# Performance work log

Measured on AMD Instinct MI355X. Metric: run time of the kernel, lower is better.

## Reference

```python
import jax, jax.numpy as jnp
import numpy as np

N_ATOMS = 8000
N_PAIRS = 80000
NF_IN = 32
NF_OUT = 32
N_DIST = 16
N_COMP = 4      # l_max=1: [l=0 (1), l=1 (3)] tensor components
N_INV = 2       # _invariant_counts[(2, 1)]
MIND_SOFT = 0.85
MAXD_SOFT = 5.0
HARD_CUTOFF = 6.5
GN_EPS = 1e-5


def _sensitivity(dist, mu, sigma):
    # HIP-NN style inverse-distance Gaussians with smooth cos^2 cutoff.
    inv_d = 1.0 / dist                                   # (P,)
    base = jnp.exp(-0.5 * ((inv_d[:, None] - mu) / sigma) ** 2)  # (P, n_dist)
    cut = jnp.where(dist < HARD_CUTOFF,
                    jnp.cos(0.5 * jnp.pi * dist / HARD_CUTOFF) ** 2, 0.0)
    return base * cut[:, None]


def setup_inputs() -> dict:
    key = jax.random.key(0)
    ks = jax.random.split(key, 10)
    in_features = jax.random.normal(ks[0], (N_ATOMS, NF_IN), jnp.float32)
    pair_first = jnp.sort(jax.random.randint(ks[1], (N_PAIRS,), 0, N_ATOMS))
    pair_second = jax.random.randint(ks[2], (N_PAIRS,), 0, N_ATOMS)
    dist_pairs = (0.5 + (HARD_CUTOFF - 0.5)
                  * jax.random.uniform(ks[3], (N_PAIRS,), jnp.float32))
    tensor_rhats = jax.random.normal(ks[4], (N_PAIRS, N_COMP), jnp.float32)
    # learned params
    sens_mu = jnp.linspace(1.0 / MAXD_SOFT, 1.0 / MIND_SOFT, N_DIST).astype(jnp.float32)
    sens_sigma = jnp.full((N_DIST,), float(sens_mu[1] - sens_mu[0]), jnp.float32)
    s_int = (2.0 / (N_DIST * NF_IN + NF_OUT)) ** 0.5
    int_weights = s_int * jax.random.normal(ks[5], (N_DIST, NF_OUT, NF_IN), jnp.float32)
    s_self = (2.0 / (NF_IN + NF_OUT)) ** 0.5
    selfint_w = s_self * jax.random.normal(ks[6], (NF_OUT, NF_IN), jnp.float32)
    selfint_b = jnp.zeros((NF_OUT,), jnp.float32)
    s_mix = (2.0 / (N_INV * NF_OUT + NF_OUT)) ** 0.5
    mixing_weights = s_mix * jax.random.normal(ks[7], (NF_OUT, N_INV, NF_OUT), jnp.float32)
    gn_weight = jnp.ones((N_INV * NF_OUT,), jnp.float32)
    gn_bias = jnp.zeros((N_INV * NF_OUT,), jnp.float32)
    return {
        "in_features": in_features, "tensor_rhats": tensor_rhats,
        "dist_pairs": dist_pairs, "int_weights": int_weights,
        "selfint_w": selfint_w, "selfint_b": selfint_b,
        "mixing_weights": mixing_weights, "gn_weight": gn_weight,
        "gn_bias": gn_bias, "sens_mu": sens_mu, "sens_sigma": sens_sigma,
        "pair_first": pair_first, "pair_second": pair_second,
    }


def reference(in_features, tensor_rhats, dist_pairs, int_weights,
              selfint_w, selfint_b, mixing_weights, gn_weight, gn_bias,
              sens_mu, sens_sigma, pair_first, pair_second):
    n_atoms = in_features.shape[0]
    # self interaction (Linear)
    self_part = in_features @ selfint_w.T + selfint_b          # (N, nf_out)
    # tensor sensitivities: (P, n_comp, n_dist) -> flat (P, n_comp*n_dist)
    sense = _sensitivity(dist_pairs, sens_mu, sens_sigma)      # (P, n_dist)
    sense_flat = (tensor_rhats[:, :, None] * sense[:, None, :]).reshape(
        -1, N_COMP * N_DIST)
    # envsum: env[a, s, f] = sum_{p: pair_first[p]=a} sense_flat[p, s] * feat[pair_second[p], f]
    feat_j = in_features[pair_second]                          # (P, nf_in)
    contrib = sense_flat[:, :, None] * feat_j[:, None, :]      # (P, S, nf_in)
    env = jax.ops.segment_sum(contrib, pair_first, num_segments=n_atoms)
    # interaction weights contraction
    w_rs = jnp.transpose(int_weights, (0, 2, 1)).reshape(N_DIST * NF_IN, NF_OUT)
    env_rs = env.reshape(n_atoms * N_COMP, N_DIST * NF_IN)
    tf = (env_rs @ w_rs).reshape(n_atoms, N_COMP, NF_OUT)
    tf = jnp.transpose(tf, (0, 2, 1))                          # (N, nf_out, n_comp)
    # HopInvariantLayer (n_max=2, l_max=1): [l=0 scalar, |l=1 vector|^2]
    invariants = jnp.stack(
        [tf[..., 0], jnp.sum(tf[..., 1:] ** 2, axis=-1)], axis=-1)  # (N, nf_out, 2)
    # GroupNorm over channels (n_inv groups of nf_out channels)
    x = jnp.transpose(invariants, (0, 2, 1))                   # (N, n_inv, nf_out)
    mean = jnp.mean(x, axis=-1, keepdims=True)
    var = jnp.var(x, axis=-1, keepdims=True)
    xn = (x - mean) / jnp.sqrt(var + GN_EPS)
    xn = xn * gn_weight.reshape(N_INV, NF_OUT) + gn_bias.reshape(N_INV, NF_OUT)
    norm_inv = jnp.transpose(xn, (0, 2, 1)).reshape(n_atoms, NF_OUT * N_INV)
    mix = norm_inv @ mixing_weights.reshape(NF_OUT * N_INV, NF_OUT)
    return mix + self_part
```

## Files before the change

kernel.cpp:

```cpp
#include <hip/hip_runtime.h>
#include <hip/hip_bf16.h>
#include <stdint.h>

#define GN_EPS 1e-5f

typedef __fp16 half2_t __attribute__((ext_vector_type(2)));
typedef __fp16 v8h __attribute__((ext_vector_type(8)));
typedef float v4f __attribute__((ext_vector_type(4)));
union U32H2 { uint32_t u; half2_t h; };
union U4V8 { uint4 u; v8h h; };

__device__ __forceinline__ float ldin(const void* p, int i, bool bf) {
    if (bf) {
        uint32_t u = (uint32_t)((const uint16_t*)p)[i];
        union { uint32_t u; float f; } c; c.u = u << 16;
        return c.f;
    }
    return ((const float*)p)[i];
}

__device__ __forceinline__ uint16_t f2bf(float x) {
    union { float f; uint32_t u; } c; c.f = x;
    uint32_t u = c.u;
    return (uint16_t)((u + 0x7FFFu + ((u >> 16) & 1u)) >> 16);
}

__device__ __forceinline__ bool detect_bf16(const void* gnw) {
    uint32_t det = *(const uint32_t*)gnw;
    return (det >> 16) == (det & 0xFFFFu);
}

__device__ __forceinline__ uint32_t pkh2(float lo, float hi) {
    U32H2 u; u.h = __builtin_amdgcn_cvt_pkrtz(lo, hi); return u.u;
}

__global__ __launch_bounds__(256) void k0_prep(
    const void* __restrict__ feat, const void* __restrict__ rhats,
    const void* __restrict__ dists, const void* __restrict__ intw,
    const void* __restrict__ selfw, const void* __restrict__ selfb,
    const void* __restrict__ mw, const void* __restrict__ gnw,
    const void* __restrict__ gnb, const void* __restrict__ mu,
    const void* __restrict__ sig, const int* __restrict__ pf,
    const int* __restrict__ ps,
    int* __restrict__ seg, uint32_t* __restrict__ Wmf,
    float* __restrict__ featf, float4* __restrict__ rc4,
    float2* __restrict__ dj2, float* __restrict__ mwf,
    float* __restrict__ selfwf, float* __restrict__ gnwf,
    float* __restrict__ gnbf, float* __restrict__ selfbf,
    float* __restrict__ muf, float* __restrict__ isgf,
    int n_atoms, int n_pairs)
{
    const bool bf = detect_bf16(gnw);
    const int tid = blockIdx.x * 256 + threadIdx.x;

    if (tid < n_pairs) {
        int a0 = pf[tid];
        if (tid == 0) { for (int a = 0; a <= a0; ++a) seg[a] = 0; }
        if (tid + 1 < n_pairs) {
            int a1 = pf[tid + 1];
            for (int a = a0 + 1; a <= a1; ++a) seg[a] = tid + 1;
        } else {
            for (int a = a0 + 1; a <= n_atoms; ++a) seg[a] = n_pairs;
        }
        float dist = ldin(dists, tid, bf);
        float cd = __cosf(0.2416609733530613f * dist);
        float cut = (dist < 6.5f) ? cd * cd : 0.0f;
        float4 rc;
        rc.x = ldin(rhats, 4 * tid + 0, bf) * cut;
        rc.y = ldin(rhats, 4 * tid + 1, bf) * cut;
        rc.z = ldin(rhats, 4 * tid + 2, bf) * cut;
        rc.w = ldin(rhats, 4 * tid + 3, bf) * cut;
        rc4[tid] = rc;
        float2 dj; dj.x = 1.0f / dist; dj.y = __int_as_float(ps[tid]);
        dj2[tid] = dj;
    }
    {
        int i0 = tid * 4;
#pragma unroll
        for (int k = 0; k < 4; ++k) {
            int i = i0 + k;
            if (i < n_atoms * 32) featf[i] = ldin(feat, i, bf);
        }
    }
    if (tid < 8192) {
        int fp = tid & 15, d = (tid >> 4) & 15, o = tid >> 8;
        float wlo = ldin(intw, (d * 32 + o) * 32 + 2 * fp, bf);
        float whi = ldin(intw, (d * 32 + o) * 32 + 2 * fp + 1, bf);
        Wmf[tid] = pkh2(wlo, whi);
    }
    if (tid < 2048) mwf[tid] = ldin(mw, tid, bf);
    if (tid < 1024) selfwf[tid] = ldin(selfw, tid, bf);
    if (tid < 64) { gnwf[tid] = ldin(gnw, tid, bf); gnbf[tid] = ldin(gnb, tid, bf); }
    if (tid < 32) selfbf[tid] = ldin(selfb, tid, bf);
    if (tid < 16) { muf[tid] = ldin(mu, tid, bf); isgf[tid] = 1.0f / ldin(sig, tid, bf); }
}

__global__ __launch_bounds__(256, 4) void k2_main(
    const int* __restrict__ seg, const uint32_t* __restrict__ Wmf,
    const float* __restrict__ featf, const float4* __restrict__ rc4,
    const float2* __restrict__ dj2, const float* __restrict__ mwf,
    const float* __restrict__ selfwf, const float* __restrict__ gnwf,
    const float* __restrict__ gnbf, const float* __restrict__ selfbf,
    const float* __restrict__ muf, const float* __restrict__ isgf,
    const void* __restrict__ gnw, void* __restrict__ out, int n_atoms)
{
    __shared__ uint32_t envs[16 * 256];
    __shared__ float tfs[4 * 32 * 4];

    const int t = threadIdx.x, wv = t >> 6, lane = t & 63;
    int a = blockIdx.x * 4 + wv;
    const bool astore = (a < n_atoms);
    if (!astore) a = n_atoms - 1;

    const int dD = lane >> 2, fq = lane & 3;
    const float mu_d = muf[dD], isg_d = isgf[dD];

    float env[4][8];
#pragma unroll
    for (int c = 0; c < 4; ++c)
#pragma unroll
        for (int fl = 0; fl < 8; ++fl) env[c][fl] = 0.0f;

    const int s = seg[a], e = seg[a + 1];

    for (int p = s; p < e; p += 4) {
        float2 dj[4]; float4 rc[4];
#pragma unroll
        for (int i = 0; i < 4; ++i) {
            int pi = (p + i < e) ? p + i : e - 1;
            dj[i] = dj2[pi];
            float4 r = rc4[pi];
            if (p + i >= e) r = make_float4(0.f, 0.f, 0.f, 0.f);
            rc[i] = r;
        }
        float4 fa[4], fb[4];
#pragma unroll
        for (int i = 0; i < 4; ++i) {
            const float4* fr = (const float4*)(featf +
                (size_t)__float_as_int(dj[i].y) * 32) + fq * 2;
            fa[i] = fr[0]; fb[i] = fr[1];
        }
#pragma unroll
        for (int i = 0; i < 4; ++i) {
            float x = (dj[i].x - mu_d) * isg_d;
            float sd = __expf(-0.5f * x * x);
            float t0 = sd * rc[i].x, t1 = sd * rc[i].y;
            float t2 = sd * rc[i].z, t3 = sd * rc[i].w;
            float fj[8] = {fa[i].x, fa[i].y, fa[i].z, fa[i].w,
                           fb[i].x, fb[i].y, fb[i].z, fb[i].w};
#pragma unroll
            for (int fl = 0; fl < 8; ++fl) {
                env[0][fl] = fmaf(t0, fj[fl], env[0][fl]);
                env[1][fl] = fmaf(t1, fj[fl], env[1][fl]);
                env[2][fl] = fmaf(t2, fj[fl], env[2][fl]);
                env[3][fl] = fmaf(t3, fj[fl], env[3][fl]);
            }
        }
    }

    {
        const int ci = dD * 4 + fq;
#pragma unroll
        for (int c = 0; c < 4; ++c) {
            int m = wv * 4 + c;
            uint4 w;
            w.x = pkh2(env[c][0], env[c][1]);
            w.y = pkh2(env[c][2], env[c][3]);
            w.z = pkh2(env[c][4], env[c][5]);
            w.w = pkh2(env[c][6], env[c][7]);
            *(uint4*)&envs[m * 256 + ((ci ^ m) << 2)] = w;
        }
    }
    __syncthreads();

    if ((wv & 1) == 0) {
        const int tile = wv >> 1;
        const int mrow = lane & 15, quad = lane >> 4;
        v4f acc = {0.f, 0.f, 0.f, 0.f};
        const uint4* wb = (const uint4*)Wmf + ((tile * 16 + mrow) * 64 + quad);
#pragma unroll
        for (int kk = 0; kk < 16; ++kk) {
            int cia = kk * 4 + quad;
            U4V8 Af, Bf;
            Af.u = *(const uint4*)&envs[mrow * 256 + ((cia ^ mrow) << 2)];
            Bf.u = wb[kk * 4];
            acc = __builtin_amdgcn_mfma_f32_16x16x32_f16(Af.h, Bf.h, acc, 0, 0, 0);
        }
        float4 st; st.x = acc[0]; st.y = acc[1]; st.z = acc[2]; st.w = acc[3];
        *(float4*)&tfs[(quad * 32 + tile * 16 + mrow) * 4] = st;
    }
    __syncthreads();

    const int o = lane & 31, half = lane >> 5;
    float4 tf = *(const float4*)&tfs[(wv * 32 + o) * 4];
    float inv0 = tf.x;
    float inv1 = tf.y * tf.y + tf.z * tf.z + tf.w * tf.w;

    float s0 = inv0, q0 = inv0 * inv0, s1 = inv1, q1 = inv1 * inv1;
#pragma unroll
    for (int m = 16; m >= 1; m >>= 1) {
        s0 += __shfl_xor(s0, m, 32);
        q0 += __shfl_xor(q0, m, 32);
        s1 += __shfl_xor(s1, m, 32);
        q1 += __shfl_xor(q1, m, 32);
    }
    float mean0 = s0 * (1.f / 32.f), mean1 = s1 * (1.f / 32.f);
    float var0 = q0 * (1.f / 32.f) - mean0 * mean0;
    float var1 = q1 * (1.f / 32.f) - mean1 * mean1;
    float xn0 = (inv0 - mean0) * rsqrtf(var0 + GN_EPS);
    float xn1 = (inv1 - mean1) * rsqrtf(var1 + GN_EPS);
    xn0 = xn0 * gnwf[o] + gnbf[o];
    xn1 = xn1 * gnwf[32 + o] + gnbf[32 + o];

    float mix = 0.0f;
#pragma unroll
    for (int k = 0; k < 64; ++k) {
        float xk = __shfl((k & 1) ? xn1 : xn0, k >> 1, 32);
        mix = fmaf(xk, mwf[k * 32 + o], mix);
    }

    float sacc = selfbf[o];
    const float4* fr4 = (const float4*)(featf + (size_t)a * 32);
    const float4* sw4 = (const float4*)(selfwf + o * 32);
#pragma unroll
    for (int k = 0; k < 8; ++k) {
        float4 fv = fr4[k], w4 = sw4[k];
        sacc = fmaf(fv.x, w4.x, sacc);
        sacc = fmaf(fv.y, w4.y, sacc);
        sacc = fmaf(fv.z, w4.z, sacc);
        sacc = fmaf(fv.w, w4.w, sacc);
    }

    float res = mix + sacc;
    if (half == 0 && astore) {
        if (detect_bf16(gnw)) ((uint16_t*)out)[a * 32 + o] = f2bf(res);
        else                  ((float*)out)[a * 32 + o]    = res;
    }
}

extern "C" void kernel_launch(void* const* d_in, const int* in_sizes, int n_in,
                              void* d_out, int out_size, void* d_ws, size_t ws_size,
                              hipStream_t stream) {
    const void* feat  = d_in[0];
    const void* rhats = d_in[1];
    const void* dists = d_in[2];
    const void* intw  = d_in[3];
    const void* selfw = d_in[4];
    const void* selfb = d_in[5];
    const void* mw    = d_in[6];
    const void* gnw   = d_in[7];
    const void* gnb   = d_in[8];
    const void* mu    = d_in[9];
    const void* sig   = d_in[10];
    const int* pf     = (const int*)d_in[11];
    const int* ps     = (const int*)d_in[12];

    const int n_pairs = in_sizes[11];
    const int n_atoms = in_sizes[0] / 32;

    char* ws = (char*)d_ws;
    int*      seg    = (int*)(ws + 0);
    uint32_t* Wmf    = (uint32_t*)(ws + 32768);
    float*    featf  = (float*)(ws + 65536);
    float4*   rc4    = (float4*)(ws + 1089536);
    float2*   dj2    = (float2*)(ws + 2369536);
    float*    mwf    = (float*)(ws + 3009536);
    float*    selfwf = (float*)(ws + 3017728);
    float*    gnwf   = (float*)(ws + 3021824);
    float*    gnbf   = (float*)(ws + 3022080);
    float*    selfbf = (float*)(ws + 3022336);
    float*    muf    = (float*)(ws + 3022464);
    float*    isgf   = (float*)(ws + 3022528);

    int thr = n_pairs;
    int feat_thr = (n_atoms * 32 + 3) / 4;
    if (feat_thr > thr) thr = feat_thr;
    if (thr < 8192) thr = 8192;
    hipLaunchKernelGGL(k0_prep, dim3((thr + 255) / 256), dim3(256), 0, stream,
                       feat, rhats, dists, intw, selfw, selfb, mw, gnw, gnb,
                       mu, sig, pf, ps, seg, Wmf, featf, rc4, dj2, mwf,
                       selfwf, gnwf, gnbf, selfbf, muf, isgf, n_atoms, n_pairs);
    hipLaunchKernelGGL(k2_main, dim3((n_atoms + 3) / 4), dim3(256), 0, stream,
                       seg, Wmf, featf, rc4, dj2, mwf, selfwf, gnwf, gnbf,
                       selfbf, muf, isgf, gnw, d_out, n_atoms);
}
```

Baseline: 119.0 us.

## Pre-gather neighbor features per pair as packed fp16 in a separate prep kernel

Splits the prep kernel into an atom/weight prep and a per-pair prep. The pair prep gathers each pair's neighbor feature row and stores it contiguously as packed fp16, so the main kernel reads features sequentially by pair index instead of through a random gather. This trades an extra kernel launch and a ~5 MB write/read stream for removing the indirect fp32 gather in the hot loop. It also lowers feature precision to fp16 in the accumulation input.

```diff
diff --git a/kernel.cpp b/kernel.cpp
--- a/kernel.cpp
+++ b/kernel.cpp
@@ -34,46 +34,20 @@
     U32H2 u; u.h = __builtin_amdgcn_cvt_pkrtz(lo, hi); return u.u;
 }
 
-__global__ __launch_bounds__(256) void k0_prep(
-    const void* __restrict__ feat, const void* __restrict__ rhats,
-    const void* __restrict__ dists, const void* __restrict__ intw,
+__global__ __launch_bounds__(256) void k0a_prep(
+    const void* __restrict__ feat, const void* __restrict__ intw,
     const void* __restrict__ selfw, const void* __restrict__ selfb,
     const void* __restrict__ mw, const void* __restrict__ gnw,
     const void* __restrict__ gnb, const void* __restrict__ mu,
-    const void* __restrict__ sig, const int* __restrict__ pf,
-    const int* __restrict__ ps,
-    int* __restrict__ seg, uint32_t* __restrict__ Wmf,
-    float* __restrict__ featf, float4* __restrict__ rc4,
-    float2* __restrict__ dj2, float* __restrict__ mwf,
-    float* __restrict__ selfwf, float* __restrict__ gnwf,
-    float* __restrict__ gnbf, float* __restrict__ selfbf,
-    float* __restrict__ muf, float* __restrict__ isgf,
-    int n_atoms, int n_pairs)
+    const void* __restrict__ sig,
+    uint32_t* __restrict__ Wmf, float* __restrict__ featf,
+    float* __restrict__ mwf, float* __restrict__ selfwf,
+    float* __restrict__ gnwf, float* __restrict__ gnbf,
+    float* __restrict__ selfbf, float* __restrict__ muf,
+    float* __restrict__ isgf, int n_atoms)
 {
     const bool bf = detect_bf16(gnw);
     const int tid = blockIdx.x * 256 + threadIdx.x;
-
-    if (tid < n_pairs) {
-        int a0 = pf[tid];
-        if (tid == 0) { for (int a = 0; a <= a0; ++a) seg[a] = 0; }
-        if (tid + 1 < n_pairs) {
-            int a1 = pf[tid + 1];
-            for (int a = a0 + 1; a <= a1; ++a) seg[a] = tid + 1;
-        } else {
-            for (int a = a0 + 1; a <= n_atoms; ++a) seg[a] = n_pairs;
-        }
-        float dist = ldin(dists, tid, bf);
-        float cd = __cosf(0.2416609733530613f * dist);
-        float cut = (dist < 6.5f) ? cd * cd : 0.0f;
-        float4 rc;
-        rc.x = ldin(rhats, 4 * tid + 0, bf) * cut;
-        rc.y = ldin(rhats, 4 * tid + 1, bf) * cut;
-        rc.z = ldin(rhats, 4 * tid + 2, bf) * cut;
-        rc.w = ldin(rhats, 4 * tid + 3, bf) * cut;
-        rc4[tid] = rc;
-        float2 dj; dj.x = 1.0f / dist; dj.y = __int_as_float(ps[tid]);
-        dj2[tid] = dj;
-    }
     {
         int i0 = tid * 4;
 #pragma unroll
@@ -95,14 +69,57 @@
     if (tid < 16) { muf[tid] = ldin(mu, tid, bf); isgf[tid] = 1.0f / ldin(sig, tid, bf); }
 }
 
+__global__ __launch_bounds__(256) void k0b_pairs(
+    const void* __restrict__ feat, const void* __restrict__ rhats,
+    const void* __restrict__ dists, const void* __restrict__ gnw,
+    const int* __restrict__ pf, const int* __restrict__ ps,
+    int* __restrict__ seg, float4* __restrict__ sp4,
+    float* __restrict__ si, uint32_t* __restrict__ fh,
+    int n_atoms, int n_pairs)
+{
+    const bool bf = detect_bf16(gnw);
+    const int tid = blockIdx.x * 256 + threadIdx.x;
+    if (tid >= n_pairs) return;
+
+    int a0 = pf[tid];
+    if (tid == 0) { for (int a = 0; a <= a0; ++a) seg[a] = 0; }
+    if (tid + 1 < n_pairs) {
+        int a1 = pf[tid + 1];
+        for (int a = a0 + 1; a <= a1; ++a) seg[a] = tid + 1;
+    } else {
+        for (int a = a0 + 1; a <= n_atoms; ++a) seg[a] = n_pairs;
+    }
+
+    float dist = ldin(dists, tid, bf);
+    float cd = __cosf(0.2416609733530613f * dist);
+    float cut = (dist < 6.5f) ? cd * cd : 0.0f;
+    float4 rc;
+    rc.x = ldin(rhats, 4 * tid + 0, bf) * cut;
+    rc.y = ldin(rhats, 4 * tid + 1, bf) * cut;
+    rc.z = ldin(rhats, 4 * tid + 2, bf) * cut;
+    rc.w = ldin(rhats, 4 * tid + 3, bf) * cut;
+    sp4[tid] = rc;
+    si[tid] = 1.0f / dist;
+
+    const int j = ps[tid];
+    uint32_t* o = fh + (size_t)tid * 16;
+#pragma unroll
+    for (int k = 0; k < 16; ++k) {
+        float lo = ldin(feat, j * 32 + 2 * k, bf);
+        float hi = ldin(feat, j * 32 + 2 * k + 1, bf);
+        o[k] = pkh2(lo, hi);
+    }
+}
+
 __global__ __launch_bounds__(256, 4) void k2_main(
     const int* __restrict__ seg, const uint32_t* __restrict__ Wmf,
-    const float* __restrict__ featf, const float4* __restrict__ rc4,
-    const float2* __restrict__ dj2, const float* __restrict__ mwf,
-    const float* __restrict__ selfwf, const float* __restrict__ gnwf,
-    const float* __restrict__ gnbf, const float* __restrict__ selfbf,
-    const float* __restrict__ muf, const float* __restrict__ isgf,
-    const void* __restrict__ gnw, void* __restrict__ out, int n_atoms)
+    const float* __restrict__ featf, const float4* __restrict__ sp4,
+    const float* __restrict__ si, const uint32_t* __restrict__ fh,
+    const float* __restrict__ mwf, const float* __restrict__ selfwf,
+    const float* __restrict__ gnwf, const float* __restrict__ gnbf,
+    const float* __restrict__ selfbf, const float* __restrict__ muf,
+    const float* __restrict__ isgf, const void* __restrict__ gnw,
+    void* __restrict__ out, int n_atoms)
 {
     __shared__ uint32_t envs[16 * 256];
     __shared__ float tfs[4 * 32 * 4];
@@ -124,30 +141,26 @@
     const int s = seg[a], e = seg[a + 1];
 
     for (int p = s; p < e; p += 4) {
-        float2 dj[4]; float4 rc[4];
+        float4 rc[4]; float invd[4]; uint4 f4[4];
 #pragma unroll
         for (int i = 0; i < 4; ++i) {
             int pi = (p + i < e) ? p + i : e - 1;
-            dj[i] = dj2[pi];
-            float4 r = rc4[pi];
+            float4 r = sp4[pi];
             if (p + i >= e) r = make_float4(0.f, 0.f, 0.f, 0.f);
             rc[i] = r;
-        }
-        float4 fa[4], fb[4];
+            invd[i] = si[pi];
+            f4[i] = *(const uint4*)(fh + (size_t)pi * 16 + fq * 4);
+        }
 #pragma unroll
         for (int i = 0; i < 4; ++i) {
-            const float4* fr = (const float4*)(featf +
-                (size_t)__float_as_int(dj[i].y) * 32) + fq * 2;
-            fa[i] = fr[0]; fb[i] = fr[1];
-        }
-#pragma unroll
-        for (int i = 0; i < 4; ++i) {
-            float x = (dj[i].x - mu_d) * isg_d;
+            float x = (invd[i] - mu_d) * isg_d;
             float sd = __expf(-0.5f * x * x);
             float t0 = sd * rc[i].x, t1 = sd * rc[i].y;
             float t2 = sd * rc[i].z, t3 = sd * rc[i].w;
-            float fj[8] = {fa[i].x, fa[i].y, fa[i].z, fa[i].w,
-                           fb[i].x, fb[i].y, fb[i].z, fb[i].w};
+            U32H2 h0, h1, h2, h3;
+            h0.u = f4[i].x; h1.u = f4[i].y; h2.u = f4[i].z; h3.u = f4[i].w;
+            float fj[8] = {(float)h0.h.x, (float)h0.h.y, (float)h1.h.x, (float)h1.h.y,
+                           (float)h2.h.x, (float)h2.h.y, (float)h3.h.x, (float)h3.h.y};
 #pragma unroll
             for (int fl = 0; fl < 8; ++fl) {
                 env[0][fl] = fmaf(t0, fj[fl], env[0][fl]);
@@ -262,25 +275,27 @@
     int*      seg    = (int*)(ws + 0);
     uint32_t* Wmf    = (uint32_t*)(ws + 32768);
     float*    featf  = (float*)(ws + 65536);
-    float4*   rc4    = (float4*)(ws + 1089536);
-    float2*   dj2    = (float2*)(ws + 2369536);
-    float*    mwf    = (float*)(ws + 3009536);
-    float*    selfwf = (float*)(ws + 3017728);
-    float*    gnwf   = (float*)(ws + 3021824);
-    float*    gnbf   = (float*)(ws + 3022080);
-    float*    selfbf = (float*)(ws + 3022336);
-    float*    muf    = (float*)(ws + 3022464);
-    float*    isgf   = (float*)(ws + 3022528);
-
-    int thr = n_pairs;
-    int feat_thr = (n_atoms * 32 + 3) / 4;
-    if (feat_thr > thr) thr = feat_thr;
-    if (thr < 8192) thr = 8192;
-    hipLaunchKernelGGL(k0_prep, dim3((thr + 255) / 256), dim3(256), 0, stream,
-                       feat, rhats, dists, intw, selfw, selfb, mw, gnw, gnb,
-                       mu, sig, pf, ps, seg, Wmf, featf, rc4, dj2, mwf,
-                       selfwf, gnwf, gnbf, selfbf, muf, isgf, n_atoms, n_pairs);
+    float4*   sp4    = (float4*)(ws + 1089536);
+    float*    si     = (float*)(ws + 2369536);
+    uint32_t* fh     = (uint32_t*)(ws + 2689536);
+    float*    mwf    = (float*)(ws + 7809536);
+    float*    selfwf = (float*)(ws + 7817728);
+    float*    gnwf   = (float*)(ws + 7821824);
+    float*    gnbf   = (float*)(ws + 7822080);
+    float*    selfbf = (float*)(ws + 7822336);
+    float*    muf    = (float*)(ws + 7822464);
+    float*    isgf   = (float*)(ws + 7822528);
+
+    int thr_a = (n_atoms * 32 + 3) / 4;
+    if (thr_a < 8192) thr_a = 8192;
+    hipLaunchKernelGGL(k0a_prep, dim3((thr_a + 255) / 256), dim3(256), 0, stream,
+                       feat, intw, selfw, selfb, mw, gnw, gnb, mu, sig,
+                       Wmf, featf, mwf, selfwf, gnwf, gnbf, selfbf, muf, isgf,
+                       n_atoms);
+    hipLaunchKernelGGL(k0b_pairs, dim3((n_pairs + 255) / 256), dim3(256), 0, stream,
+                       feat, rhats, dists, gnw, pf, ps,
+                       seg, sp4, si, fh, n_atoms, n_pairs);
     hipLaunchKernelGGL(k2_main, dim3((n_atoms + 3) / 4), dim3(256), 0, stream,
-                       seg, Wmf, featf, rc4, dj2, mwf, selfwf, gnwf, gnbf,
+                       seg, Wmf, featf, sp4, si, fh, mwf, selfwf, gnwf, gnbf,
                        selfbf, muf, isgf, gnw, d_out, n_atoms);
 }
```

Result: slower. 134.3 us (+12.8%).
